# Kernel optimization log

Hardware: AMD Instinct MI355X
Metric: run time of the kernel (lower is better)

Reference implementation:

```python
import jax, jax.numpy as jnp
import numpy as np

NEG_SLOPE = 0.2  # PyG GATConv default


def add_self_loops(edge_index, num_nodes):
    loops = jnp.arange(num_nodes, dtype=edge_index.dtype)
    return jnp.concatenate([edge_index, jnp.stack([loops, loops])], axis=1)


def gat_conv(x, edge_index, W, att_src, att_dst, bias, heads, out_ch, concat):
    # x: [N, F_in]; edge_index: [2, E] with row0=src(j), row1=dst(i)
    N = x.shape[0]
    xl = (x @ W).reshape(N, heads, out_ch)              # [N, H, C]
    src, dst = edge_index[0], edge_index[1]
    a_src = jnp.einsum('nhc,hc->nh', xl, att_src)        # [N, H]
    a_dst = jnp.einsum('nhc,hc->nh', xl, att_dst)        # [N, H]
    alpha = jax.nn.leaky_relu(a_src[src] + a_dst[dst], NEG_SLOPE)  # [E, H]
    # segment softmax over incoming edges of each dst node
    m = jax.ops.segment_max(alpha, dst, num_segments=N)  # [N, H]
    e = jnp.exp(alpha - m[dst])
    denom = jax.ops.segment_sum(e, dst, num_segments=N)
    coef = e / (denom[dst] + 1e-16)                      # [E, H]
    msg = xl[src] * coef[..., None]                      # [E, H, C]
    out = jax.ops.segment_sum(msg, dst, num_segments=N)  # [N, H, C]
    out = out.reshape(N, heads * out_ch) if concat else out.mean(axis=1)
    return out + bias


def setup_inputs() -> dict:
    key = jax.random.key(0)
    ks = jax.random.split(key, 12)
    N, E = 50000, 800000
    nfeat, nhid, nheads, nclass = 512, 8, 8, 16
    hid = nhid * nheads  # 64
    s1 = 1.0 / np.sqrt(nfeat)
    s2 = 1.0 / np.sqrt(hid)
    return {
        'x': jax.random.normal(ks[0], (N, nfeat), jnp.float32),
        'edge_index': jax.random.randint(ks[1], (2, E), 0, N, jnp.int64 if jax.config.jax_enable_x64 else jnp.int32),
        'W1': jax.random.uniform(ks[2], (nfeat, hid), jnp.float32, -s1, s1),
        'att_src1': jax.random.uniform(ks[3], (nheads, nhid), jnp.float32, -s2, s2),
        'att_dst1': jax.random.uniform(ks[4], (nheads, nhid), jnp.float32, -s2, s2),
        'bias1': jnp.zeros((hid,), jnp.float32),
        'W2': jax.random.uniform(ks[5], (hid, nclass), jnp.float32, -s2, s2),
        'att_src2': jax.random.uniform(ks[6], (1, nclass), jnp.float32, -0.25, 0.25),
        'att_dst2': jax.random.uniform(ks[7], (1, nclass), jnp.float32, -0.25, 0.25),
        'bias2': jnp.zeros((nclass,), jnp.float32),
    }


def reference(x, edge_index, W1, att_src1, att_dst1, bias1, W2, att_src2, att_dst2, bias2):
    N = x.shape[0]
    ei = add_self_loops(edge_index, N)
    # dropout layers are identity at inference
    h = gat_conv(x, ei, W1, att_src1, att_dst1, bias1, heads=8, out_ch=8, concat=True)
    o = gat_conv(h, ei, W2, att_src2, att_dst2, bias2, heads=1, out_ch=16, concat=True)
    o = jax.nn.elu(o)
    return jax.nn.log_softmax(o, axis=1)
```

## Files before the change

kernel.cpp:

```cpp
#include <hip/hip_runtime.h>
#include <math.h>

#define NEG_SLOPE 0.2f
#define PAD 64

typedef short short8 __attribute__((ext_vector_type(8)));
typedef float floatx4 __attribute__((ext_vector_type(4)));

static __device__ __forceinline__ float bf2f(unsigned short u) {
  return __uint_as_float(((unsigned int)u) << 16);
}
static __device__ __forceinline__ unsigned short f2bf(float f) {
  unsigned int u = __float_as_uint(f);
  u = (u + 0x7fffu + ((u >> 16) & 1u)) >> 16;
  return (unsigned short)u;
}

__global__ __launch_bounds__(256) void cvt_hist(const float* __restrict__ x,
                                                unsigned short* __restrict__ xb,
                                                const float* __restrict__ W1,
                                                unsigned short* __restrict__ W1t,
                                                const int* __restrict__ ei,
                                                int* __restrict__ cnt,
                                                int* __restrict__ rank,
                                                long long total, int E,
                                                int ipc, int NH) {
  int b = blockIdx.x;
  int tid = threadIdx.x;
  if (b < NH) {
    int beg = b * ipc;
    int end = min(beg + ipc, E);
    for (int i = beg + tid; i < end; i += 256) {
      int d = ei[E + i];
      rank[i] = atomicAdd(&cnt[d], 1);
    }
    return;
  }
  if (b < NH + 128) {
    int i = (b - NH) * 256 + tid;
    int k = i >> 6, c = i & 63;
    W1t[c * 512 + k] = f2bf(W1[i]);
    return;
  }
  long long base = (long long)(b - NH - 128) * 2048;
  long long i0 = base + tid * 4;
  long long i1 = base + 1024 + tid * 4;
  if (i1 + 4 <= total) {
    float4 f0 = *(const float4*)(x + i0);
    float4 f1 = *(const float4*)(x + i1);
    ushort4 u0 = make_ushort4(f2bf(f0.x), f2bf(f0.y), f2bf(f0.z), f2bf(f0.w));
    ushort4 u1 = make_ushort4(f2bf(f1.x), f2bf(f1.y), f2bf(f1.z), f2bf(f1.w));
    *(ushort4*)(xb + i0) = u0;
    *(ushort4*)(xb + i1) = u1;
  } else {
#pragma unroll
    for (int k = 0; k < 4; ++k) {
      if (i0 + k < total) xb[i0 + k] = f2bf(x[i0 + k]);
      if (i1 + k < total) xb[i1 + k] = f2bf(x[i1 + k]);
    }
  }
}

__global__ __launch_bounds__(256) void gemm1_scatter(const unsigned short* __restrict__ xb,
                                                     const unsigned short* __restrict__ W1t,
                                                     const float* __restrict__ att_src,
                                                     const float* __restrict__ att_dst,
                                                     unsigned short* __restrict__ xlb,
                                                     float* __restrict__ a_src,
                                                     float* __restrict__ a_dst, int M,
                                                     const int* __restrict__ ei,
                                                     const int* __restrict__ rank,
                                                     int* __restrict__ srcs_pad,
                                                     int E, int ipc, int NSC) {
  __shared__ unsigned short As[64 * 72];
  __shared__ unsigned short Bs[64 * 72];
  int tid = threadIdx.x;
  if ((int)blockIdx.x < NSC) {
    int total = E + M;
    int beg = blockIdx.x * ipc;
    int end = min(beg + ipc, total);
    for (int i = beg + tid; i < end; i += 256) {
      if (i < E) {
        int d = ei[E + i];
        srcs_pad[(size_t)d * PAD + 1 + rank[i]] = ei[i];
      } else {
        int n = i - E;
        srcs_pad[(size_t)n * PAD] = n;
      }
    }
    return;
  }
  int gb = blockIdx.x - NSC;
  int w = tid >> 6, lane = tid & 63;
  int q = lane >> 4, cl = lane & 15;
  int row0 = gb << 6;
  floatx4 acc[4] = {};

  int sr = tid >> 2;
  int c4 = tid & 3;
  int arow = row0 + sr;
  bool okA = arow < M;
  const unsigned short* Ap = xb + (size_t)arow * 512;
  const unsigned short* Bp = W1t + sr * 512;
  unsigned short* AsW0 = As + sr * 72 + c4 * 8;
  unsigned short* BsW0 = Bs + sr * 72 + c4 * 8;

  uint4 a0 = make_uint4(0, 0, 0, 0), a1 = a0;
  uint4 b0, b1;
  if (okA) {
    a0 = *(const uint4*)(Ap + c4 * 8);
    a1 = *(const uint4*)(Ap + 32 + c4 * 8);
  }
  b0 = *(const uint4*)(Bp + c4 * 8);
  b1 = *(const uint4*)(Bp + 32 + c4 * 8);

#pragma unroll
  for (int k0 = 0; k0 < 512; k0 += 64) {
    __syncthreads();
    *(uint4*)(AsW0)      = a0;
    *(uint4*)(AsW0 + 32) = a1;
    *(uint4*)(BsW0)      = b0;
    *(uint4*)(BsW0 + 32) = b1;
    __syncthreads();
    if (k0 < 448) {
      a0 = make_uint4(0, 0, 0, 0); a1 = a0;
      if (okA) {
        a0 = *(const uint4*)(Ap + k0 + 64 + c4 * 8);
        a1 = *(const uint4*)(Ap + k0 + 96 + c4 * 8);
      }
      b0 = *(const uint4*)(Bp + k0 + 64 + c4 * 8);
      b1 = *(const uint4*)(Bp + k0 + 96 + c4 * 8);
    }
#pragma unroll
    for (int kk = 0; kk < 2; ++kk) {
      short8 af = *(const short8*)(As + (w * 16 + cl) * 72 + kk * 32 + q * 8);
#pragma unroll
      for (int t = 0; t < 4; ++t) {
        short8 bf = *(const short8*)(Bs + (t * 16 + cl) * 72 + kk * 32 + q * 8);
        acc[t] = __builtin_amdgcn_mfma_f32_16x16x32_bf16(af, bf, acc[t], 0, 0, 0);
      }
    }
  }

  float asv[4], adv[4];
#pragma unroll
  for (int t = 0; t < 4; ++t) {
    asv[t] = att_src[t * 16 + cl];
    adv[t] = att_dst[t * 16 + cl];
  }
#pragma unroll
  for (int reg = 0; reg < 4; ++reg) {
    int r = row0 + w * 16 + q * 4 + reg;
    bool ok = r < M;
#pragma unroll
    for (int t = 0; t < 4; ++t) {
      float v = acc[t][reg];
      if (ok) xlb[(size_t)r * 64 + t * 16 + cl] = f2bf(v);
      float ps = v * asv[t];
      float pd = v * adv[t];
      ps += __shfl_xor(ps, 1); pd += __shfl_xor(pd, 1);
      ps += __shfl_xor(ps, 2); pd += __shfl_xor(pd, 2);
      ps += __shfl_xor(ps, 4); pd += __shfl_xor(pd, 4);
      if (ok && (cl & 7) == 0) {
        int h = t * 2 + (cl >> 3);
        a_src[r * 8 + h] = ps;
        a_dst[r * 8 + h] = pd;
      }
    }
  }
}

__global__ __launch_bounds__(256) void agg1_fused(const int* __restrict__ cnt,
                                                  const int* __restrict__ srcs,
                                                  const float* __restrict__ a_src,
                                                  const float* __restrict__ a_dst,
                                                  const unsigned short* __restrict__ xlb,
                                                  const float* __restrict__ bias1,
                                                  const float* __restrict__ W2,
                                                  const float* __restrict__ att_src2,
                                                  const float* __restrict__ att_dst2,
                                                  float* __restrict__ xl2,
                                                  float* __restrict__ a_src2,
                                                  float* __restrict__ a_dst2, int N) {
  __shared__ float W2s[64 * 16];
  __shared__ float hsm[4][64];
  int tid = threadIdx.x;
  W2s[tid]       = W2[tid];
  W2s[tid + 256] = W2[tid + 256];
  W2s[tid + 512] = W2[tid + 512];
  W2s[tid + 768] = W2[tid + 768];
  __syncthreads();

  int wv = tid >> 6, lane = tid & 63;
  int node = (blockIdx.x << 2) + wv;
  if (node >= N) return;
  int half = lane >> 5;
  int j = lane & 31;
  int h = j >> 2;
  int beg = node * PAD;
  int end = beg + 1 + cnt[node];
  float ad = a_dst[node * 8 + h];
  float den = 0.f, acc0 = 0.f, acc1 = 0.f;

  int p = beg + half;
  bool v0 = p < end,      v1 = p + 2 < end,  v2 = p + 4 < end,  v3 = p + 6 < end;
  bool v4 = p + 8 < end,  v5 = p + 10 < end, v6 = p + 12 < end, v7 = p + 14 < end;
  int s0 = srcs[v0 ? p : beg];
  int s1 = srcs[v1 ? p + 2 : beg];
  int s2 = srcs[v2 ? p + 4 : beg];
  int s3 = srcs[v3 ? p + 6 : beg];
  int s4 = srcs[v4 ? p + 8 : beg];
  int s5 = srcs[v5 ? p + 10 : beg];
  int s6 = srcs[v6 ? p + 12 : beg];
  int s7 = srcs[v7 ? p + 14 : beg];
  while (v0) {
    int np = p + 16;
    bool u0 = np < end,      u1 = np + 2 < end,  u2 = np + 4 < end,  u3 = np + 6 < end;
    bool u4 = np + 8 < end,  u5 = np + 10 < end, u6 = np + 12 < end, u7 = np + 14 < end;
    int t0 = srcs[u0 ? np : beg];
    int t1 = srcs[u1 ? np + 2 : beg];
    int t2 = srcs[u2 ? np + 4 : beg];
    int t3 = srcs[u3 ? np + 6 : beg];
    int t4 = srcs[u4 ? np + 8 : beg];
    int t5 = srcs[u5 ? np + 10 : beg];
    int t6 = srcs[u6 ? np + 12 : beg];
    int t7 = srcs[u7 ? np + 14 : beg];
    float a0 = a_src[s0 * 8 + h] + ad;
    float a1 = a_src[s1 * 8 + h] + ad;
    float a2 = a_src[s2 * 8 + h] + ad;
    float a3 = a_src[s3 * 8 + h] + ad;
    float a4 = a_src[s4 * 8 + h] + ad;
    float a5 = a_src[s5 * 8 + h] + ad;
    float a6 = a_src[s6 * 8 + h] + ad;
    float a7 = a_src[s7 * 8 + h] + ad;
    ushort2 x0 = *(const ushort2*)(xlb + (size_t)s0 * 64 + 2 * j);
    ushort2 x1 = *(const ushort2*)(xlb + (size_t)s1 * 64 + 2 * j);
    ushort2 x2 = *(const ushort2*)(xlb + (size_t)s2 * 64 + 2 * j);
    ushort2 x3 = *(const ushort2*)(xlb + (size_t)s3 * 64 + 2 * j);
    ushort2 x4 = *(const ushort2*)(xlb + (size_t)s4 * 64 + 2 * j);
    ushort2 x5 = *(const ushort2*)(xlb + (size_t)s5 * 64 + 2 * j);
    ushort2 x6 = *(const ushort2*)(xlb + (size_t)s6 * 64 + 2 * j);
    ushort2 x7 = *(const ushort2*)(xlb + (size_t)s7 * 64 + 2 * j);
    a0 = a0 >= 0.f ? a0 : NEG_SLOPE * a0;
    a1 = a1 >= 0.f ? a1 : NEG_SLOPE * a1;
    a2 = a2 >= 0.f ? a2 : NEG_SLOPE * a2;
    a3 = a3 >= 0.f ? a3 : NEG_SLOPE * a3;
    a4 = a4 >= 0.f ? a4 : NEG_SLOPE * a4;
    a5 = a5 >= 0.f ? a5 : NEG_SLOPE * a5;
    a6 = a6 >= 0.f ? a6 : NEG_SLOPE * a6;
    a7 = a7 >= 0.f ? a7 : NEG_SLOPE * a7;
    float w0 = v0 ? __expf(a0) : 0.f;
    float w1 = v1 ? __expf(a1) : 0.f;
    float w2 = v2 ? __expf(a2) : 0.f;
    float w3 = v3 ? __expf(a3) : 0.f;
    float w4 = v4 ? __expf(a4) : 0.f;
    float w5 = v5 ? __expf(a5) : 0.f;
    float w6 = v6 ? __expf(a6) : 0.f;
    float w7 = v7 ? __expf(a7) : 0.f;
    den += ((w0 + w1) + (w2 + w3)) + ((w4 + w5) + (w6 + w7));
    acc0 += (w0 * bf2f(x0.x) + w1 * bf2f(x1.x)) + (w2 * bf2f(x2.x) + w3 * bf2f(x3.x)) +
            (w4 * bf2f(x4.x) + w5 * bf2f(x5.x)) + (w6 * bf2f(x6.x) + w7 * bf2f(x7.x));
    acc1 += (w0 * bf2f(x0.y) + w1 * bf2f(x1.y)) + (w2 * bf2f(x2.y) + w3 * bf2f(x3.y)) +
            (w4 * bf2f(x4.y) + w5 * bf2f(x5.y)) + (w6 * bf2f(x6.y) + w7 * bf2f(x7.y));
    p = np;
    s0 = t0; s1 = t1; s2 = t2; s3 = t3; s4 = t4; s5 = t5; s6 = t6; s7 = t7;
    v0 = u0; v1 = u1; v2 = u2; v3 = u3; v4 = u4; v5 = u5; v6 = u6; v7 = u7;
  }
  den  += __shfl_xor(den, 32);
  acc0 += __shfl_xor(acc0, 32);
  acc1 += __shfl_xor(acc1, 32);
  float inv = 1.f / (den + 1e-16f);
  float2 bv = *(const float2*)(bias1 + 2 * j);
  float h0 = acc0 * inv + bv.x;
  float h1 = acc1 * inv + bv.y;
  if (half == 0) {
    hsm[wv][2 * j]     = h0;
    hsm[wv][2 * j + 1] = h1;
  }
  if (lane < 16) {
    float sum = 0.f;
#pragma unroll
    for (int k = 0; k < 64; ++k) sum += hsm[wv][k] * W2s[k * 16 + lane];
    xl2[(size_t)node * 16 + lane] = sum;
    float ps = sum * att_src2[lane];
    float pd = sum * att_dst2[lane];
#pragma unroll
    for (int w = 8; w >= 1; w >>= 1) {
      ps += __shfl_xor(ps, w, 16);
      pd += __shfl_xor(pd, w, 16);
    }
    if (lane == 0) { a_src2[node] = ps; a_dst2[node] = pd; }
  }
}

__global__ __launch_bounds__(256) void agg2_fin(const int* __restrict__ cnt,
                                                const int* __restrict__ srcs,
                                                const float* __restrict__ a_src2,
                                                const float* __restrict__ a_dst2,
                                                const float* __restrict__ xl2,
                                                const float* __restrict__ bias2,
                                                float* __restrict__ out, int N) {
  int t = blockIdx.x * blockDim.x + threadIdx.x;
  int node = t >> 4;
  int c = t & 15;
  if (node >= N) return;
  int beg = node * PAD;
  int end = beg + 1 + cnt[node];
  float ad = a_dst2[node];
  float den = 0.f, acc = 0.f;
  int p = beg;
  bool v0 = true,          v1 = p + 1 < end, v2 = p + 2 < end, v3 = p + 3 < end;
  bool v4 = p + 4 < end,   v5 = p + 5 < end, v6 = p + 6 < end, v7 = p + 7 < end;
  int s0 = srcs[p];
  int s1 = srcs[v1 ? p + 1 : beg];
  int s2 = srcs[v2 ? p + 2 : beg];
  int s3 = srcs[v3 ? p + 3 : beg];
  int s4 = srcs[v4 ? p + 4 : beg];
  int s5 = srcs[v5 ? p + 5 : beg];
  int s6 = srcs[v6 ? p + 6 : beg];
  int s7 = srcs[v7 ? p + 7 : beg];
  while (v0) {
    int np = p + 8;
    bool u0 = np < end,     u1 = np + 1 < end, u2 = np + 2 < end, u3 = np + 3 < end;
    bool u4 = np + 4 < end, u5 = np + 5 < end, u6 = np + 6 < end, u7 = np + 7 < end;
    int t0 = srcs[u0 ? np : beg];
    int t1 = srcs[u1 ? np + 1 : beg];
    int t2 = srcs[u2 ? np + 2 : beg];
    int t3 = srcs[u3 ? np + 3 : beg];
    int t4 = srcs[u4 ? np + 4 : beg];
    int t5 = srcs[u5 ? np + 5 : beg];
    int t6 = srcs[u6 ? np + 6 : beg];
    int t7 = srcs[u7 ? np + 7 : beg];
    float a0 = a_src2[s0] + ad, a1 = a_src2[s1] + ad;
    float a2 = a_src2[s2] + ad, a3 = a_src2[s3] + ad;
    float a4 = a_src2[s4] + ad, a5 = a_src2[s5] + ad;
    float a6 = a_src2[s6] + ad, a7 = a_src2[s7] + ad;
    float x0 = xl2[(size_t)s0 * 16 + c], x1 = xl2[(size_t)s1 * 16 + c];
    float x2 = xl2[(size_t)s2 * 16 + c], x3 = xl2[(size_t)s3 * 16 + c];
    float x4 = xl2[(size_t)s4 * 16 + c], x5 = xl2[(size_t)s5 * 16 + c];
    float x6 = xl2[(size_t)s6 * 16 + c], x7 = xl2[(size_t)s7 * 16 + c];
    a0 = a0 >= 0.f ? a0 : NEG_SLOPE * a0;
    a1 = a1 >= 0.f ? a1 : NEG_SLOPE * a1;
    a2 = a2 >= 0.f ? a2 : NEG_SLOPE * a2;
    a3 = a3 >= 0.f ? a3 : NEG_SLOPE * a3;
    a4 = a4 >= 0.f ? a4 : NEG_SLOPE * a4;
    a5 = a5 >= 0.f ? a5 : NEG_SLOPE * a5;
    a6 = a6 >= 0.f ? a6 : NEG_SLOPE * a6;
    a7 = a7 >= 0.f ? a7 : NEG_SLOPE * a7;
    float w0 = v0 ? __expf(a0) : 0.f;
    float w1 = v1 ? __expf(a1) : 0.f;
    float w2 = v2 ? __expf(a2) : 0.f;
    float w3 = v3 ? __expf(a3) : 0.f;
    float w4 = v4 ? __expf(a4) : 0.f;
    float w5 = v5 ? __expf(a5) : 0.f;
    float w6 = v6 ? __expf(a6) : 0.f;
    float w7 = v7 ? __expf(a7) : 0.f;
    den += ((w0 + w1) + (w2 + w3)) + ((w4 + w5) + (w6 + w7));
    acc += (w0 * x0 + w1 * x1) + (w2 * x2 + w3 * x3) +
           (w4 * x4 + w5 * x5) + (w6 * x6 + w7 * x7);
    p = np;
    s0 = t0; s1 = t1; s2 = t2; s3 = t3; s4 = t4; s5 = t5; s6 = t6; s7 = t7;
    v0 = u0; v1 = u1; v2 = u2; v3 = u3; v4 = u4; v5 = u5; v6 = u6; v7 = u7;
  }
  float o = acc / (den + 1e-16f) + bias2[c];
  o = o > 0.f ? o : expm1f(o);
  float mx = o;
#pragma unroll
  for (int w = 8; w >= 1; w >>= 1) mx = fmaxf(mx, __shfl_xor(mx, w, 16));
  float e = __expf(o - mx);
  float ssum = e;
#pragma unroll
  for (int w = 8; w >= 1; w >>= 1) ssum += __shfl_xor(ssum, w, 16);
  out[(size_t)node * 16 + c] = o - mx - logf(ssum);
}

static inline size_t rnd16(size_t x) { return (x + 15) & ~(size_t)15; }

extern "C" void kernel_launch(void* const* d_in, const int* in_sizes, int n_in,
                              void* d_out, int out_size, void* d_ws, size_t ws_size,
                              hipStream_t stream) {
  const float* x        = (const float*)d_in[0];
  const int*   ei       = (const int*)d_in[1];
  const float* W1       = (const float*)d_in[2];
  const float* att_src1 = (const float*)d_in[3];
  const float* att_dst1 = (const float*)d_in[4];
  const float* bias1    = (const float*)d_in[5];
  const float* W2       = (const float*)d_in[6];
  const float* att_src2 = (const float*)d_in[7];
  const float* att_dst2 = (const float*)d_in[8];
  const float* bias2    = (const float*)d_in[9];
  float* out = (float*)d_out;

  int N = in_sizes[0] / 512;
  int E = in_sizes[1] / 2;

  char* ws = (char*)d_ws;
  unsigned short* xb  = (unsigned short*)ws;  ws += rnd16((size_t)N * 512 * 2);
  unsigned short* xlb = (unsigned short*)ws;  ws += rnd16((size_t)N * 64 * 2);
  unsigned short* W1t = (unsigned short*)ws;  ws += rnd16((size_t)512 * 64 * 2);
  float* a_src1 = (float*)ws;                 ws += rnd16((size_t)N * 8 * 4);
  float* a_dst1 = (float*)ws;                 ws += rnd16((size_t)N * 8 * 4);
  float* xl2    = (float*)ws;                 ws += rnd16((size_t)N * 16 * 4);
  float* a_src2 = (float*)ws;                 ws += rnd16((size_t)N * 4);
  float* a_dst2 = (float*)ws;                 ws += rnd16((size_t)N * 4);
  int* cnt      = (int*)ws;                   ws += rnd16((size_t)N * 4);
  int* rank     = (int*)ws;                   ws += rnd16((size_t)E * 4);
  int* srcs_pad = (int*)ws;                   ws += rnd16((size_t)N * PAD * 4);

  const int NH  = 256;
  const int NSC = 256;
  long long total = (long long)N * 512;
  int GC = (int)((total + 2047) / 2048);
  int G1 = (N + 63) / 64;
  int ipc_h = (E + NH - 1) / NH;
  int ipc_s = (E + N + NSC - 1) / NSC;

  hipMemsetAsync(cnt, 0, (size_t)N * sizeof(int), stream);
  cvt_hist<<<NH + 128 + GC, 256, 0, stream>>>(x, xb, W1, W1t, ei, cnt, rank,
                                              total, E, ipc_h, NH);
  gemm1_scatter<<<NSC + G1, 256, 0, stream>>>(xb, W1t, att_src1, att_dst1,
                                              xlb, a_src1, a_dst1, N,
                                              ei, rank, srcs_pad, E, ipc_s, NSC);
  agg1_fused<<<(N + 3) / 4, 256, 0, stream>>>(cnt, srcs_pad, a_src1, a_dst1, xlb,
                                              bias1, W2, att_src2, att_dst2,
                                              xl2, a_src2, a_dst2, N);
  agg2_fin<<<((size_t)N * 16 + 255) / 256, 256, 0, stream>>>(cnt, srcs_pad, a_src2, a_dst2,
                                                             xl2, bias2, out, N);
}
```

Measured before the change: 274.0 us.

## Replace global-atomic degree histogram with chunked LDS histograms plus prefix pass

Result: slower. 293.3 us (+7.0%).

```diff
diff --git a/kernel.cpp b/kernel.cpp
--- a/kernel.cpp
+++ b/kernel.cpp
@@ -3,6 +3,9 @@
 
 #define NEG_SLOPE 0.2f
 #define PAD 64
+#define NCHUNKS 64
+#define HWORDS 12800
+#define TWORDS 25600
 
 typedef short short8 __attribute__((ext_vector_type(8)));
 typedef float floatx4 __attribute__((ext_vector_type(4)));
@@ -16,33 +19,65 @@
   return (unsigned short)u;
 }
 
-__global__ __launch_bounds__(256) void cvt_hist(const float* __restrict__ x,
-                                                unsigned short* __restrict__ xb,
-                                                const float* __restrict__ W1,
-                                                unsigned short* __restrict__ W1t,
-                                                const int* __restrict__ ei,
-                                                int* __restrict__ cnt,
-                                                int* __restrict__ rank,
-                                                long long total, int E,
-                                                int ipc, int NH) {
+__global__ __launch_bounds__(256) void lds_hist(const int* __restrict__ ei,
+                                                unsigned short* __restrict__ rank_local,
+                                                unsigned int* __restrict__ bcnt,
+                                                int E, int ipc) {
+  __shared__ unsigned int lcnt[HWORDS];
+  int c = blockIdx.x >> 1, h = blockIdx.x & 1;
+  int tid = threadIdx.x;
+  for (int w = tid; w < HWORDS; w += 256) lcnt[w] = 0;
+  __syncthreads();
+  int nlo = h * (HWORDS * 2);
+  int beg = c * ipc, end = min(beg + ipc, E);
+  for (int i = beg + tid; i < end; i += 256) {
+    int d = ei[E + i];
+    unsigned int dn = (unsigned int)(d - nlo);
+    if (dn < (unsigned int)(HWORDS * 2)) {
+      unsigned int sh = (dn & 1u) * 16u;
+      unsigned int old = atomicAdd(&lcnt[dn >> 1], 1u << sh);
+      rank_local[i] = (unsigned short)((old >> sh) & 0xFFFFu);
+    }
+  }
+  __syncthreads();
+  unsigned int* dst = bcnt + (size_t)c * TWORDS + h * HWORDS;
+  for (int w = tid; w < HWORDS; w += 256) dst[w] = lcnt[w];
+}
+
+__global__ __launch_bounds__(256) void cvt_prefix(const float* __restrict__ x,
+                                                  unsigned short* __restrict__ xb,
+                                                  const float* __restrict__ W1,
+                                                  unsigned short* __restrict__ W1t,
+                                                  unsigned int* __restrict__ bcnt,
+                                                  int* __restrict__ cnt,
+                                                  long long total, int N, int NPB) {
   int b = blockIdx.x;
   int tid = threadIdx.x;
-  if (b < NH) {
-    int beg = b * ipc;
-    int end = min(beg + ipc, E);
-    for (int i = beg + tid; i < end; i += 256) {
-      int d = ei[E + i];
-      rank[i] = atomicAdd(&cnt[d], 1);
+  if (b < NPB) {
+    int w = b * 256 + tid;
+    if (w < TWORDS) {
+      unsigned int r0 = 0, r1 = 0;
+#pragma unroll 4
+      for (int c = 0; c < NCHUNKS; ++c) {
+        size_t idx = (size_t)c * TWORDS + w;
+        unsigned int v = bcnt[idx];
+        bcnt[idx] = r0 | (r1 << 16);
+        r0 += v & 0xFFFFu;
+        r1 += v >> 16;
+      }
+      int n0 = 2 * w, n1 = 2 * w + 1;
+      if (n0 < N) cnt[n0] = (int)r0;
+      if (n1 < N) cnt[n1] = (int)r1;
     }
     return;
   }
-  if (b < NH + 128) {
-    int i = (b - NH) * 256 + tid;
-    int k = i >> 6, c = i & 63;
-    W1t[c * 512 + k] = f2bf(W1[i]);
+  if (b < NPB + 128) {
+    int i = (b - NPB) * 256 + tid;
+    int k = i >> 6, cc = i & 63;
+    W1t[cc * 512 + k] = f2bf(W1[i]);
     return;
   }
-  long long base = (long long)(b - NH - 128) * 2048;
+  long long base = (long long)(b - NPB - 128) * 2048;
   long long i0 = base + tid * 4;
   long long i1 = base + 1024 + tid * 4;
   if (i1 + 4 <= total) {
@@ -69,9 +104,10 @@
                                                      float* __restrict__ a_src,
                                                      float* __restrict__ a_dst, int M,
                                                      const int* __restrict__ ei,
-                                                     const int* __restrict__ rank,
+                                                     const unsigned short* __restrict__ rank_local,
+                                                     const unsigned int* __restrict__ bcnt,
                                                      int* __restrict__ srcs_pad,
-                                                     int E, int ipc, int NSC) {
+                                                     int E, int ipc_h, int ipc, int NSC) {
   __shared__ unsigned short As[64 * 72];
   __shared__ unsigned short Bs[64 * 72];
   int tid = threadIdx.x;
@@ -82,7 +118,10 @@
     for (int i = beg + tid; i < end; i += 256) {
       if (i < E) {
         int d = ei[E + i];
-        srcs_pad[(size_t)d * PAD + 1 + rank[i]] = ei[i];
+        int c = i / ipc_h;
+        unsigned int bw = bcnt[(size_t)c * TWORDS + (d >> 1)];
+        int base = (int)((bw >> ((d & 1) * 16)) & 0xFFFFu);
+        srcs_pad[(size_t)d * PAD + 1 + base + rank_local[i]] = ei[i];
       } else {
         int n = i - E;
         srcs_pad[(size_t)n * PAD] = n;
@@ -404,23 +443,25 @@
   float* a_src2 = (float*)ws;                 ws += rnd16((size_t)N * 4);
   float* a_dst2 = (float*)ws;                 ws += rnd16((size_t)N * 4);
   int* cnt      = (int*)ws;                   ws += rnd16((size_t)N * 4);
-  int* rank     = (int*)ws;                   ws += rnd16((size_t)E * 4);
+  unsigned int* bcnt = (unsigned int*)ws;     ws += rnd16((size_t)NCHUNKS * TWORDS * 4);
+  unsigned short* rank_local = (unsigned short*)ws; ws += rnd16((size_t)E * 2);
   int* srcs_pad = (int*)ws;                   ws += rnd16((size_t)N * PAD * 4);
 
-  const int NH  = 256;
+  const int NPB = 100;
   const int NSC = 256;
   long long total = (long long)N * 512;
   int GC = (int)((total + 2047) / 2048);
   int G1 = (N + 63) / 64;
-  int ipc_h = (E + NH - 1) / NH;
+  int ipc_h = (E + NCHUNKS - 1) / NCHUNKS;
   int ipc_s = (E + N + NSC - 1) / NSC;
 
-  hipMemsetAsync(cnt, 0, (size_t)N * sizeof(int), stream);
-  cvt_hist<<<NH + 128 + GC, 256, 0, stream>>>(x, xb, W1, W1t, ei, cnt, rank,
-                                              total, E, ipc_h, NH);
+  lds_hist<<<NCHUNKS * 2, 256, 0, stream>>>(ei, rank_local, bcnt, E, ipc_h);
+  cvt_prefix<<<NPB + 128 + GC, 256, 0, stream>>>(x, xb, W1, W1t, bcnt, cnt,
+                                                 total, N, NPB);
   gemm1_scatter<<<NSC + G1, 256, 0, stream>>>(xb, W1t, att_src1, att_dst1,
                                               xlb, a_src1, a_dst1, N,
-                                              ei, rank, srcs_pad, E, ipc_s, NSC);
+                                              ei, rank_local, bcnt, srcs_pad,
+                                              E, ipc_h, ipc_s, NSC);
   agg1_fused<<<(N + 3) / 4, 256, 0, stream>>>(cnt, srcs_pad, a_src1, a_dst1, xlb,
                                               bias1, W2, att_src2, att_dst2,
                                               xl2, a_src2, a_dst2, N);
```
